# Performance work log

Hardware: AMD Instinct MI355X
Metric: run time of the kernel (lower is better)

The kernel has to match this reference:

```python
import jax, jax.numpy as jnp
import numpy as np

NUM_SAMPLES = 8192   # num_parallel_samples
HIDDEN = 512
EMB = 40             # embedding_dim(10) * freq_map['H'](4)
C_IN = 1
TIME_FEAT = 4
HIST_LEN = 336
PRED_LEN = 48
MIN_SCALE = 1e-5
SAMPLE_KEY_SEED = 42


def _gru_cell(h, x, W_ih, W_hh, b_ih, b_hh):
    # torch GRU cell: gates stacked as [r, z, n] along rows of W (each HIDDEN)
    gi = x @ W_ih.T + b_ih            # [B, 3H]
    gh = h @ W_hh.T + b_hh            # [B, 3H]
    H = h.shape[-1]
    i_r, i_z, i_n = gi[:, :H], gi[:, H:2 * H], gi[:, 2 * H:]
    h_r, h_z, h_n = gh[:, :H], gh[:, H:2 * H], gh[:, 2 * H:]
    r = jax.nn.sigmoid(i_r + h_r)
    z = jax.nn.sigmoid(i_z + h_z)
    n = jnp.tanh(i_n + r * h_n)
    return (1.0 - z) * n + z * h


def setup_inputs() -> dict:
    key = jax.random.key(0)
    ks = jax.random.split(key, 16)
    f32 = jnp.float32
    inp = {
        "x": jax.random.normal(ks[0], (1, HIST_LEN, C_IN), dtype=f32),
        "x_mark": jax.random.normal(ks[1], (1, HIST_LEN, TIME_FEAT), dtype=f32),
        "y_mark": jax.random.normal(ks[2], (1, PRED_LEN, TIME_FEAT), dtype=f32),
        "mode": 0,
        # time_feat_embedding: Linear(4 -> 40), torch layout [out, in]
        "W_emb": jax.random.normal(ks[3], (EMB, TIME_FEAT), dtype=f32) * 0.05,
        "b_emb": jnp.zeros((EMB,), dtype=f32),
        # GRU (1 layer): input size = c_in + EMB = 41
        "W_ih": jax.random.normal(ks[4], (3 * HIDDEN, C_IN + EMB), dtype=f32) * 0.05,
        "W_hh": jax.random.normal(ks[5], (3 * HIDDEN, HIDDEN), dtype=f32) * 0.05,
        "b_ih": jnp.zeros((3 * HIDDEN,), dtype=f32),
        "b_hh": jnp.zeros((3 * HIDDEN,), dtype=f32),
        # StudentT args projection: three Linear(HIDDEN -> 1)
        "W_df": jax.random.normal(ks[6], (1, HIDDEN), dtype=f32) * 0.05,
        "b_df": jnp.zeros((1,), dtype=f32),
        "W_loc": jax.random.normal(ks[7], (1, HIDDEN), dtype=f32) * 0.05,
        "b_loc": jnp.zeros((1,), dtype=f32),
        "W_sc": jax.random.normal(ks[8], (1, HIDDEN), dtype=f32) * 0.05,
        "b_sc": jnp.zeros((1,), dtype=f32),
    }
    return inp


def _deepar_sample(x, x_mark, y_mark, W_emb, b_emb, W_ih, W_hh, b_ih, b_hh,
                   W_df, b_df, W_loc, b_loc, W_sc, b_sc):
    S = NUM_SAMPLES
    # ---- encoder (unroll_encoder with y=None) ----
    scale = jnp.clip(jnp.mean(jnp.abs(x), axis=1, keepdims=True), MIN_SCALE, None)  # [1,1,1]
    seq = x / scale
    tfe = x_mark @ W_emb.T + b_emb                      # [1, T, EMB]
    enc_in = jnp.concatenate([seq, tfe], axis=-1)       # [1, T, 41]
    h0 = jnp.zeros((1, HIDDEN), dtype=x.dtype)

    def enc_step(h, xt):  # xt: [1, 41]
        h = _gru_cell(h, xt, W_ih, W_hh, b_ih, b_hh)
        return h, None

    h_T, _ = jax.lax.scan(enc_step, h0, jnp.swapaxes(enc_in, 0, 1))  # [1, H]

    # ---- sampling decoder ----
    h = jnp.broadcast_to(h_T, (S, HIDDEN))              # repeat state across samples
    # note: original feeds the UNSCALED last observation as first decoder input
    tgt0 = jnp.broadcast_to(x[0, -1, :], (S, C_IN))     # [S, 1]
    emb_y = y_mark[0] @ W_emb.T + b_emb                 # [pred_len, EMB]
    scale_s = scale[0, 0, 0]                            # scalar (batch=1, c=1)
    base_key = jax.random.key(SAMPLE_KEY_SEED)

    def dec_step(carry, xs):
        h, tgt = carry
        e_k, k = xs
        inp = jnp.concatenate([tgt, jnp.broadcast_to(e_k, (S, EMB))], axis=-1)  # [S, 41]
        h = _gru_cell(h, inp, W_ih, W_hh, b_ih, b_hh)
        # StudentTOutput domain map: df = 2 + softplus, loc raw, scale = softplus
        df = 2.0 + jax.nn.softplus(h @ W_df.T + b_df)   # [S, 1]
        loc = h @ W_loc.T + b_loc                       # [S, 1]
        sc = jax.nn.softplus(h @ W_sc.T + b_sc)         # [S, 1]
        eps = jax.random.t(jax.random.fold_in(base_key, k),
                           jax.lax.stop_gradient(df), df.shape, dtype=df.dtype)
        sample = (loc + sc * eps) * scale_s             # AffineTransformed(scale)
        return (h, sample), sample

    ks = jnp.arange(PRED_LEN)
    _, samples = jax.lax.scan(dec_step, (h, tgt0), (emb_y, ks))  # [pred_len, S, 1]
    return jnp.transpose(samples, (1, 0, 2))            # [S, pred_len, c_out]


def reference(x, x_mark, y_mark, mode, W_emb, b_emb, W_ih, W_hh, b_ih, b_hh,
              W_df, b_df, W_loc, b_loc, W_sc, b_sc):
    # mode=0 -> sampling/inference path (the kernel target)
    return _deepar_sample(x, x_mark, y_mark, W_emb, b_emb, W_ih, W_hh, b_ih, b_hh,
                          W_df, b_df, W_loc, b_loc, W_sc, b_sc)
```

## Files before the change

### kernel.cpp

```cpp
#include <hip/hip_runtime.h>
#include <cmath>


#define JAX_PARTITIONABLE 1

#define HIDDEN 512
#define EMB 40
#define HIST 336
#define PRED 48
#define S_N 8192
#define ENC_BLOCKS 48

#define HPLANE (8192 * 512)
#define WPLANE (1536 * 512)
#define INV4096 (1.0f / 4096.0f)

typedef __attribute__((ext_vector_type(8))) _Float16 half8;
typedef __attribute__((ext_vector_type(4))) float f32x4;

struct KeyPair { unsigned a, b; };

__device__ __forceinline__ unsigned rotl32_(unsigned v, unsigned s) {
  return (v << s) | (v >> (32u - s));
}

__device__ __forceinline__ KeyPair tf2x32(KeyPair k, unsigned x0, unsigned x1) {
  unsigned ks0 = k.a, ks1 = k.b, ks2 = ks0 ^ ks1 ^ 0x1BD11BDAu;
  x0 += ks0; x1 += ks1;
#define TF_R(r) { x0 += x1; x1 = rotl32_(x1, r); x1 ^= x0; }
  TF_R(13u) TF_R(15u) TF_R(26u) TF_R(6u)  x0 += ks1; x1 += ks2 + 1u;
  TF_R(17u) TF_R(29u) TF_R(16u) TF_R(24u) x0 += ks2; x1 += ks0 + 2u;
  TF_R(13u) TF_R(15u) TF_R(26u) TF_R(6u)  x0 += ks0; x1 += ks1 + 3u;
  TF_R(17u) TF_R(29u) TF_R(16u) TF_R(24u) x0 += ks1; x1 += ks2 + 4u;
  TF_R(13u) TF_R(15u) TF_R(26u) TF_R(6u)  x0 += ks2; x1 += ks0 + 5u;
#undef TF_R
  KeyPair r; r.a = x0; r.b = x1; return r;
}

__device__ __forceinline__ void split2_(KeyPair key, KeyPair& r0, KeyPair& r1) {
#if JAX_PARTITIONABLE
  r0 = tf2x32(key, 0u, 0u);
  r1 = tf2x32(key, 0u, 1u);
#else
  KeyPair p0 = tf2x32(key, 0u, 2u);
  KeyPair p1 = tf2x32(key, 1u, 3u);
  r0.a = p0.a; r0.b = p1.a;
  r1.a = p0.b; r1.b = p1.b;
#endif
}

__device__ __forceinline__ void split3_(KeyPair key, KeyPair& r0, KeyPair& r1, KeyPair& r2) {
#if JAX_PARTITIONABLE
  r0 = tf2x32(key, 0u, 0u);
  r1 = tf2x32(key, 0u, 1u);
  r2 = tf2x32(key, 0u, 2u);
#else
  KeyPair p0 = tf2x32(key, 0u, 3u);
  KeyPair p1 = tf2x32(key, 1u, 4u);
  KeyPair p2 = tf2x32(key, 2u, 5u);
  r0.a = p0.a; r0.b = p1.a;
  r1.a = p2.a; r1.b = p0.b;
  r2.a = p1.b; r2.b = p2.b;
#endif
}

__device__ __forceinline__ unsigned scalar_bits_(KeyPair key) {
#if JAX_PARTITIONABLE
  KeyPair p = tf2x32(key, 0u, 0u);
  return p.a ^ p.b;
#else
  return tf2x32(key, 0u, 0u).a;
#endif
}

__device__ __forceinline__ unsigned batch_bits_8192_(KeyPair key, int s) {
#if JAX_PARTITIONABLE
  KeyPair p = tf2x32(key, 0u, (unsigned)s);
  return p.a ^ p.b;
#else
  if (s < 4096) return tf2x32(key, (unsigned)s, (unsigned)(4096 + s)).a;
  return tf2x32(key, (unsigned)(s - 4096), (unsigned)s).b;
#endif
}

__device__ __forceinline__ KeyPair subkey_of_8192_(KeyPair key, int s) {
#if JAX_PARTITIONABLE
  return tf2x32(key, 0u, (unsigned)s);
#else
  KeyPair r;
  if (s < 4096) {
    r.a = tf2x32(key, (unsigned)(2 * s),     (unsigned)(8192 + 2 * s)).a;
    r.b = tf2x32(key, (unsigned)(2 * s + 1), (unsigned)(8192 + 2 * s + 1)).a;
  } else {
    int m = 2 * s - 8192;
    r.a = tf2x32(key, (unsigned)m,       (unsigned)(m + 8192)).b;
    r.b = tf2x32(key, (unsigned)(m + 1), (unsigned)(m + 1 + 8192)).b;
  }
  return r;
#endif
}

__device__ __forceinline__ float acc_logf_(float x) {
  return (float)log((double)x);
}
__device__ __forceinline__ float acc_expf_(float x) {
  return (float)exp((double)x);
}

__device__ __forceinline__ float bits_to_uniform01_(unsigned bits) {
  return __uint_as_float((bits >> 9) | 0x3F800000u) - 1.0f;
}

__device__ __forceinline__ float xla_log1pf_(float t) {
  #pragma clang fp contract(off)
  float small_ = (1.0f + (-0.5f) * t) * t;
  float large_ = acc_logf_(t + 1.0f);
  return (fabsf(t) < 1e-4f) ? small_ : large_;
}

__device__ float xla_erfinv_(float x) {
  #pragma clang fp contract(off)
  float w = -xla_log1pf_(-(x * x));
  float p;
  if (w < 5.0f) {
    float ww = w - 2.5f;
    p = 2.81022636e-08f;
    p = 3.43273939e-07f + p * ww;
    p = -3.5233877e-06f + p * ww;
    p = -4.39150654e-06f + p * ww;
    p = 0.00021858087f + p * ww;
    p = -0.00125372503f + p * ww;
    p = -0.00417768164f + p * ww;
    p = 0.246640727f + p * ww;
    p = 1.50140941f + p * ww;
  } else {
    float ww = sqrtf(w) - 3.0f;
    p = -0.000200214257f;
    p = 0.000100950558f + p * ww;
    p = 0.00134934322f + p * ww;
    p = -0.00367342844f + p * ww;
    p = 0.00573950773f + p * ww;
    p = -0.0076224613f + p * ww;
    p = 0.00943887047f + p * ww;
    p = 1.00167406f + p * ww;
    p = 2.83297682f + p * ww;
  }
  return p * x;
}

__device__ float bits_to_normal_(unsigned bits) {
  #pragma clang fp contract(off)
  const float lo = __uint_as_float(0xBF7FFFFFu);
  float f = bits_to_uniform01_(bits);
  float u = f * 2.0f + lo;
  u = fmaxf(lo, u);
  return __uint_as_float(0x3FB504F3u) * xla_erfinv_(u);
}

__device__ __forceinline__ float softplus_(float x) {
  #pragma clang fp contract(off)
  float amax = fmaxf(x, 0.0f);
  float e = acc_expf_(-fabsf(x));
  return amax + xla_log1pf_(e);
}

__device__ __forceinline__ float sigmoid_(float v) { return 1.0f / (1.0f + expf(-v)); }

__device__ __forceinline__ unsigned short f2h_(float f) {
  _Float16 h = (_Float16)f;
  return __builtin_bit_cast(unsigned short, h);
}
__device__ __forceinline__ float h2f_(unsigned short b) {
  return (float)__builtin_bit_cast(_Float16, b);
}

__device__ float gamma_sample_(KeyPair gkey, float alpha) {
  #pragma clang fp contract(off)
  const float third = 0.33333334f;
  float d = alpha - third;
  float c = third / sqrtf(d);
  KeyPair key, boost_sub;
  split2_(gkey, key, boost_sub);
  (void)boost_sub;
  float X = 0.0f, V = 1.0f, U = 2.0f;
  for (int guard = 0; guard < 1024; guard++) {
    float X2 = X * X;
    float sq = 1.0f - 0.0331f * (X2 * X2);
    bool cont = false;
    if (U >= sq) {
      float lhs = acc_logf_(U);
      float rhs = (X * 0.5f) + (d * ((1.0f - V) + acc_logf_(V)));
      cont = (lhs >= rhs);
    }
    if (!cont) break;
    KeyPair nkey, xkey, Ukey;
    split3_(key, nkey, xkey, Ukey);
    key = nkey;
    float x, v;
    KeyPair kk = xkey;
    do {
      KeyPair knew, sub;
      split2_(kk, knew, sub);
      kk = knew;
      x = bits_to_normal_(scalar_bits_(sub));
      v = 1.0f + x * c;
    } while (v <= 0.0f);
    X = x * x;
    V = (v * v) * v;
    U = bits_to_uniform01_(scalar_bits_(Ukey));
  }
  return d * V;
}

__device__ float sample_t_eps_(int k, int s, float df) {
  #pragma clang fp contract(off)
  KeyPair base; base.a = 0u; base.b = 42u;
  KeyPair tkey = tf2x32(base, 0u, (unsigned)k);
  KeyPair key_n, key_g;
  split2_(tkey, key_n, key_g);
  float n = bits_to_normal_(batch_bits_8192_(key_n, s));
  KeyPair gkey = subkey_of_8192_(key_g, s);
  float half_df = df * 0.5f;
  float g = gamma_sample_(gkey, half_df);
  return n * sqrtf(half_df / g);
}


__global__ __launch_bounds__(256) void prep_kernel(
    const float* __restrict__ x, const float* __restrict__ x_mark,
    const float* __restrict__ y_mark, const float* __restrict__ W_emb,
    const float* __restrict__ b_emb, float* __restrict__ scale_p,
    float* __restrict__ tfe, float* __restrict__ emb_y,
    unsigned long long* __restrict__ gh2) {
  __shared__ float xs[HIST];
  int tid = threadIdx.x;
  for (int i = tid; i < HIST; i += 256) xs[i] = fabsf(x[i]);
  __syncthreads();
  if (tid == 0) {
    float s = 0.0f;
    for (int t = 0; t < HIST; t++) s += xs[t];
    float m = s / 336.0f;
    scale_p[0] = fmaxf(m, 1e-5f);
  }
  for (int i = tid; i < 2 * 1536; i += 256) gh2[i] = 0ull;
  for (int idx = tid; idx < HIST * EMB; idx += 256) {
    int t = idx / EMB, e = idx % EMB;
    float a = b_emb[e];
    for (int f = 0; f < 4; f++) a += x_mark[t * 4 + f] * W_emb[e * 4 + f];
    tfe[idx] = a;
  }
  for (int idx = tid; idx < PRED * EMB; idx += 256) {
    int kk = idx / EMB, e = idx % EMB;
    float a = b_emb[e];
    for (int f = 0; f < 4; f++) a += y_mark[kk * 4 + f] * W_emb[e * 4 + f];
    emb_y[idx] = a;
  }
}

__global__ __launch_bounds__(256) void enc_gi_kernel(
    const float* __restrict__ x, const float* __restrict__ tfe,
    const float* __restrict__ W_ih, const float* __restrict__ b_ih,
    const float* __restrict__ scale_p, float* __restrict__ enc_gi) {
  __shared__ float fe[EMB];
  __shared__ float xs_s;
  int t = blockIdx.x;
  int tid = threadIdx.x;
  if (tid < EMB) fe[tid] = tfe[t * EMB + tid];
  if (tid == 0) xs_s = x[t] / scale_p[0];
  __syncthreads();
  float xs = xs_s;
  for (int r = tid; r < 3 * HIDDEN; r += 256) {
    const float* wr = W_ih + (size_t)r * 41;
    float a = b_ih[r] + wr[0] * xs;
    #pragma unroll
    for (int e = 0; e < EMB; e++) a += wr[1 + e] * fe[e];
    enc_gi[(size_t)t * 1536 + r] = a;
  }
}

__global__ __launch_bounds__(256) void giy_kernel(
    const float* __restrict__ emb_y, const float* __restrict__ W_ih,
    const float* __restrict__ b_ih, float* __restrict__ giy) {
  __shared__ float fe[EMB];
  int k = blockIdx.x;
  int tid = threadIdx.x;
  if (tid < EMB) fe[tid] = emb_y[k * EMB + tid];
  __syncthreads();
  for (int r = tid; r < 3 * HIDDEN; r += 256) {
    const float* wr = W_ih + (size_t)r * 41;
    float a = b_ih[r];
    #pragma unroll
    for (int e = 0; e < EMB; e++) a += wr[1 + e] * fe[e];
    giy[(size_t)k * 1536 + r] = a;
  }
}

__global__ __launch_bounds__(256) void wsplit_kernel(
    const float* __restrict__ W_hh, unsigned short* __restrict__ Wr) {
  int row = blockIdx.x;
  int g = row >> 9;
  int jg = row & 511;
  int jb = jg >> 5, jl = jg & 31;
  size_t dst = ((size_t)jb * 96 + g * 32 + jl) * 512;
  for (int k = threadIdx.x; k < 512; k += 256) {
    float w = W_hh[(size_t)row * 512 + k];
    unsigned short g0 = f2h_(w);
    float r1 = (w - h2f_(g0)) * 4096.0f;
    unsigned short g1 = f2h_(r1);
    Wr[dst + k] = g0;
    Wr[WPLANE + dst + k] = g1;
  }
}

__global__ __launch_bounds__(256) void hsplit_kernel(
    const float* __restrict__ h_T, unsigned short* __restrict__ sT) {
  int i = threadIdx.x;
  for (int j = i; j < 512; j += 256) {
    float v = h_T[j];
    unsigned short f0 = f2h_(v);
    float r1 = (v - h2f_(f0)) * 4096.0f;
    sT[j] = f0;
    sT[512 + j] = f2h_(r1);
  }
}

__global__ __launch_bounds__(128) void h2bcast_kernel(
    const unsigned short* __restrict__ sT, unsigned short* __restrict__ h2) {
  int row = blockIdx.x;
  int tid = threadIdx.x;
  int sp = tid >> 6, c = tid & 63;
  ((uint4*)(h2 + (size_t)sp * HPLANE + (size_t)row * 512))[c] =
      ((const uint4*)(sT + sp * 512))[c];
}

__device__ __forceinline__ int hpad_(int j) { return (j >> 6) * 68 + (j & 63); }

__global__ __launch_bounds__(256) void enc_gru_kernel(
    const float* __restrict__ enc_gi, const float* __restrict__ W_hh,
    const float* __restrict__ b_hh, unsigned long long* __restrict__ gh2,
    float* __restrict__ h_T) {
  __shared__ __align__(16) float hsb[2][544];
  int tid = threadIdx.x;
  int gtid = blockIdx.x * 256 + tid;
  int row = gtid >> 3;
  int sub = gtid & 7;

  float w[64];
  const float* wp = W_hh + (size_t)row * HIDDEN + sub * 64;
  #pragma unroll
  for (int i = 0; i < 16; i++) {
    float4 v = *(const float4*)(wp + 4 * i);
    w[4 * i + 0] = v.x; w[4 * i + 1] = v.y; w[4 * i + 2] = v.z; w[4 * i + 3] = v.w;
  }
  for (int i = tid; i < 544; i += 256) hsb[0][i] = 0.f;
  float bhr0 = b_hh[tid],       bhz0 = b_hh[512 + tid],  bhn0 = b_hh[1024 + tid];
  float bhr1 = b_hh[256 + tid], bhz1 = b_hh[768 + tid],  bhn1 = b_hh[1280 + tid];
  __syncthreads();

  for (int t = 0; t < HIST; t++) {
    int par = t & 1;
    unsigned tag = (unsigned)(t + 1);
    const float* hc = hsb[par];
    float* hw = hsb[par ^ 1];

    const float* gi = enc_gi + (size_t)t * 1536;
    float gir0 = gi[tid],        giz0 = gi[512 + tid],  gin0 = gi[1024 + tid];
    float gir1 = gi[256 + tid],  giz1 = gi[768 + tid],  gin1 = gi[1280 + tid];

    float p = 0.0f;
    const float4* hv = (const float4*)(hc + sub * 68);
    #pragma unroll
    for (int i = 0; i < 16; i++) {
      float4 v = hv[i];
      p += w[4 * i + 0] * v.x + w[4 * i + 1] * v.y +
           w[4 * i + 2] * v.z + w[4 * i + 3] * v.w;
    }
    p += __shfl_xor(p, 1, 64);
    p += __shfl_xor(p, 2, 64);
    p += __shfl_xor(p, 4, 64);
    if (sub == 0) {
      unsigned long long pk =
          ((unsigned long long)tag << 32) | (unsigned long long)__float_as_uint(p);
      __hip_atomic_store(&gh2[par * 1536 + row], pk, __ATOMIC_RELAXED,
                         __HIP_MEMORY_SCOPE_AGENT);
    }

    const unsigned long long* g = gh2 + par * 1536;
    unsigned long long v0, v1, v2, v3, v4, v5;
    for (;;) {
      v0 = __hip_atomic_load(&g[tid],         __ATOMIC_RELAXED, __HIP_MEMORY_SCOPE_AGENT);
      v1 = __hip_atomic_load(&g[512 + tid],   __ATOMIC_RELAXED, __HIP_MEMORY_SCOPE_AGENT);
      v2 = __hip_atomic_load(&g[1024 + tid],  __ATOMIC_RELAXED, __HIP_MEMORY_SCOPE_AGENT);
      v3 = __hip_atomic_load(&g[256 + tid],   __ATOMIC_RELAXED, __HIP_MEMORY_SCOPE_AGENT);
      v4 = __hip_atomic_load(&g[768 + tid],   __ATOMIC_RELAXED, __HIP_MEMORY_SCOPE_AGENT);
      v5 = __hip_atomic_load(&g[1280 + tid],  __ATOMIC_RELAXED, __HIP_MEMORY_SCOPE_AGENT);
      if ((unsigned)(v0 >> 32) == tag && (unsigned)(v1 >> 32) == tag &&
          (unsigned)(v2 >> 32) == tag && (unsigned)(v3 >> 32) == tag &&
          (unsigned)(v4 >> 32) == tag && (unsigned)(v5 >> 32) == tag)
        break;
      __builtin_amdgcn_s_sleep(1);
    }

    {
      float ghr = __uint_as_float((unsigned)v0);
      float ghz = __uint_as_float((unsigned)v1);
      float ghn = __uint_as_float((unsigned)v2);
      float r = sigmoid_(gir0 + (ghr + bhr0));
      float z = sigmoid_(giz0 + (ghz + bhz0));
      float n = tanhf(gin0 + r * (ghn + bhn0));
      hw[hpad_(tid)] = (1.0f - z) * n + z * hc[hpad_(tid)];
    }
    {
      float ghr = __uint_as_float((unsigned)v3);
      float ghz = __uint_as_float((unsigned)v4);
      float ghn = __uint_as_float((unsigned)v5);
      float r = sigmoid_(gir1 + (ghr + bhr1));
      float z = sigmoid_(giz1 + (ghz + bhz1));
      float n = tanhf(gin1 + r * (ghn + bhn1));
      hw[hpad_(tid + 256)] = (1.0f - z) * n + z * hc[hpad_(tid + 256)];
    }
    __syncthreads();
  }
  if (blockIdx.x == 0) {
    h_T[tid] = hsb[0][hpad_(tid)];
    h_T[tid + 256] = hsb[0][hpad_(tid + 256)];
  }
}

__global__ __launch_bounds__(256, 2) void dec_gru_mfma(
    const unsigned short* __restrict__ h2_in,
    const unsigned short* __restrict__ Wr,
    const float* __restrict__ giy_k, const float* __restrict__ b_hh,
    const float* __restrict__ W_ih, const float* __restrict__ tgt,
    int tgt_is_x, unsigned short* __restrict__ h2_out,
    const float* __restrict__ W_df, const float* __restrict__ W_loc,
    const float* __restrict__ W_sc, float* __restrict__ partials) {
  __shared__ unsigned short As[2][2][128][32];
  int b_ = blockIdx.x;
  int xcd = b_ & 7, slot = b_ >> 3;
  int mb = xcd * 8 + (slot & 7);
  int jb = slot >> 3;
  int tid = threadIdx.x;
  int lane = tid & 63;
  int wave = tid >> 6;
  int wm = wave >> 1, wn = wave & 1;
  int s0 = mb * 128;
  int q = lane >> 4, c = lane & 15;

  f32x4 accm[4][3], accc[4][3];
  #pragma unroll
  for (int i = 0; i < 4; i++)
    #pragma unroll
    for (int g = 0; g < 3; g++) {
      accm[i][g] = (f32x4){0.f, 0.f, 0.f, 0.f};
      accc[i][g] = (f32x4){0.f, 0.f, 0.f, 0.f};
    }

  float hold[4][4];
  #pragma unroll
  for (int i = 0; i < 4; i++)
    #pragma unroll
    for (int r = 0; r < 4; r++) hold[i][r] = 0.f;

  int asp[4], arow[4], acol[4];
  #pragma unroll
  for (int r = 0; r < 4; r++) {
    int a = r * 256 + tid;
    asp[r] = a >> 9;
    int rem = a & 511;
    arow[r] = rem >> 2;
    acol[r] = rem & 3;
  }

  const unsigned short* Bbase =
      Wr + ((size_t)jb * 96 + wn * 16 + c) * 512 + q * 8;

  #pragma unroll
  for (int r = 0; r < 4; r++) {
    uint4 v = *(const uint4*)(h2_in + (size_t)asp[r] * HPLANE +
                              (size_t)(s0 + arow[r]) * 512 + acol[r] * 8);
    *(uint4*)&As[0][asp[r]][arow[r]][(acol[r] ^ (arow[r] & 3)) * 8] = v;
  }
  half8 Bcur[3][2];
  #pragma unroll
  for (int g = 0; g < 3; g++) {
    Bcur[g][0] = *(const half8*)(Bbase + (size_t)g * 32 * 512);
    Bcur[g][1] = *(const half8*)(Bbase + WPLANE + (size_t)g * 32 * 512);
  }
  __syncthreads();

  int cur = 0;
  for (int kbi = 0; kbi < 16; kbi++) {
    int kb = kbi * 32;
    uint4 Areg[4];
    half8 Bn[3][2];
    if (kbi < 15) {
      #pragma unroll
      for (int r = 0; r < 4; r++)
        Areg[r] = *(const uint4*)(h2_in + (size_t)asp[r] * HPLANE +
                                  (size_t)(s0 + arow[r]) * 512 + kb + 32 +
                                  acol[r] * 8);
      #pragma unroll
      for (int g = 0; g < 3; g++) {
        Bn[g][0] = *(const half8*)(Bbase + (size_t)g * 32 * 512 + kb + 32);
        Bn[g][1] = *(const half8*)(Bbase + WPLANE + (size_t)g * 32 * 512 + kb + 32);
      }
    }
    if (kbi == jb) {
      int cc = wn * 16 + c;
      #pragma unroll
      for (int i = 0; i < 4; i++)
        #pragma unroll
        for (int reg = 0; reg < 4; reg++) {
          int m = wm * 64 + i * 16 + q * 4 + reg;
          int idx = (((cc >> 3) ^ (m & 3)) << 3) + (cc & 7);
          hold[i][reg] = h2f_(As[cur][0][m][idx]) +
                         h2f_(As[cur][1][m][idx]) * INV4096;
        }
    }
    #pragma unroll
    for (int i = 0; i < 4; i++) {
      int m = wm * 64 + i * 16 + c;
      half8 a0 = *(const half8*)&As[cur][0][m][(q ^ (c & 3)) * 8];
      half8 a1 = *(const half8*)&As[cur][1][m][(q ^ (c & 3)) * 8];
      #pragma unroll
      for (int g = 0; g < 3; g++) {
        accm[i][g] = __builtin_amdgcn_mfma_f32_16x16x32_f16(a0, Bcur[g][0], accm[i][g], 0, 0, 0);
        accc[i][g] = __builtin_amdgcn_mfma_f32_16x16x32_f16(a0, Bcur[g][1], accc[i][g], 0, 0, 0);
        accc[i][g] = __builtin_amdgcn_mfma_f32_16x16x32_f16(a1, Bcur[g][0], accc[i][g], 0, 0, 0);
      }
    }
    if (kbi < 15) {
      #pragma unroll
      for (int r = 0; r < 4; r++)
        *(uint4*)&As[cur ^ 1][asp[r]][arow[r]][(acol[r] ^ (arow[r] & 3)) * 8] =
            Areg[r];
      #pragma unroll
      for (int g = 0; g < 3; g++) {
        Bcur[g][0] = Bn[g][0];
        Bcur[g][1] = Bn[g][1];
      }
    }
    __syncthreads();
    cur ^= 1;
  }

  float* pb = (float*)&As[0][0][0][0];
  {
    int j = jb * 32 + wn * 16 + c;
    float gyr = giy_k[j], gyz = giy_k[512 + j], gyn = giy_k[1024 + j];
    float w0r = W_ih[(size_t)j * 41];
    float w0z = W_ih[(size_t)(512 + j) * 41];
    float w0n = W_ih[(size_t)(1024 + j) * 41];
    float bhr = b_hh[j], bhz = b_hh[512 + j], bhn = b_hh[1024 + j];
    float wdj = W_df[j], wlj = W_loc[j], wsj = W_sc[j];
    #pragma unroll
    for (int i = 0; i < 4; i++) {
      #pragma unroll
      for (int reg = 0; reg < 4; reg++) {
        int s = s0 + wm * 64 + i * 16 + q * 4 + reg;
        float tg = tgt_is_x ? tgt[HIST - 1] : tgt[s];
        size_t off = (size_t)s * 512 + j;
        float h_old = hold[i][reg];
        float ghr = accm[i][0][reg] + accc[i][0][reg] * INV4096;
        float ghz = accm[i][1][reg] + accc[i][1][reg] * INV4096;
        float ghn = accm[i][2][reg] + accc[i][2][reg] * INV4096;
        float gr = (gyr + w0r * tg) + (ghr + bhr);
        float gz = (gyz + w0z * tg) + (ghz + bhz);
        float gn_i = gyn + w0n * tg;
        float gn_h = ghn + bhn;
        float r_ = sigmoid_(gr);
        float z_ = sigmoid_(gz);
        float n_ = tanhf(gn_i + r_ * gn_h);
        float hn = (1.0f - z_) * n_ + z_ * h_old;
        unsigned short f0 = f2h_(hn);
        float r1 = (hn - h2f_(f0)) * 4096.0f;
        __builtin_nontemporal_store(f0, &h2_out[off]);
        __builtin_nontemporal_store(f2h_(r1), &h2_out[HPLANE + off]);
        float vd = hn * wdj, vl = hn * wlj, vs = hn * wsj;
        #pragma unroll
        for (int o = 1; o < 16; o <<= 1) {
          vd += __shfl_xor(vd, o, 64);
          vl += __shfl_xor(vl, o, 64);
          vs += __shfl_xor(vs, o, 64);
        }
        if (c == 0) {
          int sl = i * 16 + q * 4 + reg;
          int bix = ((wm * 2 + wn) * 64 + sl) * 3;
          pb[bix + 0] = vd; pb[bix + 1] = vl; pb[bix + 2] = vs;
        }
      }
    }
  }
  __syncthreads();
  if (tid < 128) {
    int wmh = tid >> 6, sl = tid & 63;
    int ia = (wmh * 2 + 0) * 192 + sl * 3;
    int ib = ia + 192;
    int s = s0 + wmh * 64 + sl;
    size_t pofs = (size_t)s * 48 + jb * 3;
    partials[pofs + 0] = pb[ia + 0] + pb[ib + 0];
    partials[pofs + 1] = pb[ia + 1] + pb[ib + 1];
    partials[pofs + 2] = pb[ia + 2] + pb[ib + 2];
  }
}

__global__ __launch_bounds__(64) void dec_head_kernel(
    const float* __restrict__ partials, const float* __restrict__ b_df,
    const float* __restrict__ b_loc, const float* __restrict__ b_sc,
    const float* __restrict__ scale_p, float* __restrict__ tgt,
    float* __restrict__ out, int k) {
  #pragma clang fp contract(off)
  int s = blockIdx.x * 64 + threadIdx.x;
  const float* p = partials + (size_t)s * 48;
  float adf = 0.f, alo = 0.f, asc = 0.f;
  #pragma unroll
  for (int jb = 0; jb < 16; jb++) {
    adf += p[jb * 3 + 0];
    alo += p[jb * 3 + 1];
    asc += p[jb * 3 + 2];
  }
  float df = 2.0f + softplus_(adf + b_df[0]);
  float loc = alo + b_loc[0];
  float sc = softplus_(asc + b_sc[0]);
  float eps = sample_t_eps_(k, s, df);
  float smp = (loc + sc * eps) * scale_p[0];
  out[(size_t)s * PRED + k] = smp;
  tgt[s] = smp;
}

extern "C" void kernel_launch(void* const* d_in, const int* in_sizes, int n_in,
                              void* d_out, int out_size, void* d_ws, size_t ws_size,
                              hipStream_t stream) {
  const float* x      = (const float*)d_in[0];
  const float* x_mark = (const float*)d_in[1];
  const float* y_mark = (const float*)d_in[2];
  const float* W_emb  = (const float*)d_in[4];
  const float* b_emb  = (const float*)d_in[5];
  const float* W_ih   = (const float*)d_in[6];
  const float* W_hh   = (const float*)d_in[7];
  const float* b_ih   = (const float*)d_in[8];
  const float* b_hh   = (const float*)d_in[9];
  const float* W_df   = (const float*)d_in[10];
  const float* b_df   = (const float*)d_in[11];
  const float* W_loc  = (const float*)d_in[12];
  const float* b_loc  = (const float*)d_in[13];
  const float* W_sc   = (const float*)d_in[14];
  const float* b_sc   = (const float*)d_in[15];
  float* out = (float*)d_out;

  float* w = (float*)d_ws;
  unsigned short* h2_a = (unsigned short*)(w);
  unsigned short* h2_b = (unsigned short*)(w + 4194304);
  unsigned short* Wr   = (unsigned short*)(w + 8388608);
  float* enc_gi = w + 9175040;
  float* giy    = w + 9691136;
  float* tfe    = w + 9764864;
  float* emb_y  = w + 9778304;
  unsigned long long* gh2 = (unsigned long long*)(w + 9780224);
  float* h_T    = w + 9786368;
  unsigned short* sT = (unsigned short*)(w + 9786880);
  float* tgt    = w + 9787392;
  float* scale_p = w + 9795584;
  float* partials = w + 9795588;

  prep_kernel<<<1, 256, 0, stream>>>(x, x_mark, y_mark, W_emb, b_emb,
                                     scale_p, tfe, emb_y, gh2);
  enc_gi_kernel<<<HIST, 256, 0, stream>>>(x, tfe, W_ih, b_ih, scale_p, enc_gi);
  giy_kernel<<<PRED, 256, 0, stream>>>(emb_y, W_ih, b_ih, giy);
  wsplit_kernel<<<1536, 256, 0, stream>>>(W_hh, Wr);
  enc_gru_kernel<<<ENC_BLOCKS, 256, 0, stream>>>(enc_gi, W_hh, b_hh, gh2, h_T);
  hsplit_kernel<<<1, 256, 0, stream>>>(h_T, sT);
  h2bcast_kernel<<<S_N, 128, 0, stream>>>(sT, h2_a);

  for (int k = 0; k < PRED; k++) {
    const unsigned short* h_in = (k % 2 == 0) ? h2_a : h2_b;
    unsigned short* h_o = (k % 2 == 0) ? h2_b : h2_a;
    dec_gru_mfma<<<1024, 256, 0, stream>>>(
        h_in, Wr, giy + (size_t)k * 1536, b_hh, W_ih,
        (k == 0) ? x : tgt, (k == 0) ? 1 : 0, h_o,
        W_df, W_loc, W_sc, partials);
    dec_head_kernel<<<S_N / 64, 64, 0, stream>>>(
        partials, b_df, b_loc, b_sc, scale_p, tgt, out, k);
  }
}
```

Before: 5.034 ms.

## Fuse decoder steps into one persistent kernel with grid barrier and tagged targets

Replaces the 96 per-step launches (GRU MFMA step plus head kernel) with a single persistent kernel of 512 blocks. Each block handles two tiles per step and meets the others at a software grid barrier built from arrive flags and a go flag. The head/sampling phase for step k-1 runs on 32 blocks at the start of step k and publishes targets tagged with the step index. GRU blocks spin on those tags only after their matmul, which overlaps the head with the recurrent GEMM. This removes launch overhead and inter-kernel gaps, but it relies on all 512 blocks being co-resident (2 per CU) and adds spin-wait traffic.

Result: slower. 6.960 ms (+38.3%).

```diff
diff --git a/kernel.cpp b/kernel.cpp
--- a/kernel.cpp
+++ b/kernel.cpp
@@ -10,6 +10,7 @@
 #define PRED 48
 #define S_N 8192
 #define ENC_BLOCKS 48
+#define DEC_BLOCKS 512
 
 #define HPLANE (8192 * 512)
 #define WPLANE (1536 * 512)
@@ -231,7 +232,10 @@
     const float* __restrict__ y_mark, const float* __restrict__ W_emb,
     const float* __restrict__ b_emb, float* __restrict__ scale_p,
     float* __restrict__ tfe, float* __restrict__ emb_y,
-    unsigned long long* __restrict__ gh2) {
+    unsigned long long* __restrict__ gh2,
+    unsigned long long* __restrict__ tgt2,
+    unsigned long long* __restrict__ arrive,
+    unsigned long long* __restrict__ goflag) {
   __shared__ float xs[HIST];
   int tid = threadIdx.x;
   for (int i = tid; i < HIST; i += 256) xs[i] = fabsf(x[i]);
@@ -243,6 +247,9 @@
     scale_p[0] = fmaxf(m, 1e-5f);
   }
   for (int i = tid; i < 2 * 1536; i += 256) gh2[i] = 0ull;
+  for (int i = tid; i < S_N; i += 256) tgt2[i] = 0ull;
+  for (int i = tid; i < DEC_BLOCKS; i += 256) arrive[i] = 0ull;
+  if (tid == 0) goflag[0] = 0ull;
   for (int idx = tid; idx < HIST * EMB; idx += 256) {
     int t = idx / EMB, e = idx % EMB;
     float a = b_emb[e];
@@ -427,16 +434,14 @@
   }
 }
 
-__global__ __launch_bounds__(256, 2) void dec_gru_mfma(
-    const unsigned short* __restrict__ h2_in,
-    const unsigned short* __restrict__ Wr,
-    const float* __restrict__ giy_k, const float* __restrict__ b_hh,
-    const float* __restrict__ W_ih, const float* __restrict__ tgt,
-    int tgt_is_x, unsigned short* __restrict__ h2_out,
-    const float* __restrict__ W_df, const float* __restrict__ W_loc,
-    const float* __restrict__ W_sc, float* __restrict__ partials) {
-  __shared__ unsigned short As[2][2][128][32];
-  int b_ = blockIdx.x;
+__device__ void dec_slot_(
+    int b_, int k, const unsigned short* __restrict__ h2_in,
+    const unsigned short* __restrict__ Wr, const float* __restrict__ giy_k,
+    const float* __restrict__ b_hh, const float* __restrict__ W_ih,
+    float xlast, const unsigned long long* __restrict__ tgt2,
+    unsigned short* __restrict__ h2_out, const float* __restrict__ W_df,
+    const float* __restrict__ W_loc, const float* __restrict__ W_sc,
+    float* __restrict__ partials, unsigned short (*As)[2][128][32]) {
   int xcd = b_ & 7, slot = b_ >> 3;
   int mb = xcd * 8 + (slot & 7);
   int jb = slot >> 3;
@@ -543,6 +548,31 @@
     }
     __syncthreads();
     cur ^= 1;
+  }
+
+  float tgv[4][4];
+  if (k == 0) {
+    #pragma unroll
+    for (int i = 0; i < 4; i++)
+      #pragma unroll
+      for (int reg = 0; reg < 4; reg++) tgv[i][reg] = xlast;
+  } else {
+    unsigned tagk = (unsigned)k;
+    for (;;) {
+      bool ok = true;
+      #pragma unroll
+      for (int i = 0; i < 4; i++)
+        #pragma unroll
+        for (int reg = 0; reg < 4; reg++) {
+          int s = s0 + wm * 64 + i * 16 + q * 4 + reg;
+          unsigned long long v = __hip_atomic_load(&tgt2[s], __ATOMIC_RELAXED,
+                                                   __HIP_MEMORY_SCOPE_AGENT);
+          ok &= ((unsigned)(v >> 32) == tagk);
+          tgv[i][reg] = __uint_as_float((unsigned)v);
+        }
+      if (ok) break;
+      __builtin_amdgcn_s_sleep(1);
+    }
   }
 
   float* pb = (float*)&As[0][0][0][0];
@@ -559,7 +589,7 @@
       #pragma unroll
       for (int reg = 0; reg < 4; reg++) {
         int s = s0 + wm * 64 + i * 16 + q * 4 + reg;
-        float tg = tgt_is_x ? tgt[HIST - 1] : tgt[s];
+        float tg = tgv[i][reg];
         size_t off = (size_t)s * 512 + j;
         float h_old = hold[i][reg];
         float ghr = accm[i][0][reg] + accc[i][0][reg] * INV4096;
@@ -605,20 +635,20 @@
   }
 }
 
-__global__ __launch_bounds__(64) void dec_head_kernel(
-    const float* __restrict__ partials, const float* __restrict__ b_df,
-    const float* __restrict__ b_loc, const float* __restrict__ b_sc,
-    const float* __restrict__ scale_p, float* __restrict__ tgt,
-    float* __restrict__ out, int k) {
+__device__ void head_phase_(
+    int p, int tid, int k, const float* __restrict__ partials,
+    const float* __restrict__ b_df, const float* __restrict__ b_loc,
+    const float* __restrict__ b_sc, const float* __restrict__ scale_p,
+    unsigned long long* __restrict__ tgt2, float* __restrict__ out) {
   #pragma clang fp contract(off)
-  int s = blockIdx.x * 64 + threadIdx.x;
-  const float* p = partials + (size_t)s * 48;
+  int s = p * 256 + tid;
+  const float* pp = partials + (size_t)s * 48;
   float adf = 0.f, alo = 0.f, asc = 0.f;
   #pragma unroll
   for (int jb = 0; jb < 16; jb++) {
-    adf += p[jb * 3 + 0];
-    alo += p[jb * 3 + 1];
-    asc += p[jb * 3 + 2];
+    adf += pp[jb * 3 + 0];
+    alo += pp[jb * 3 + 1];
+    asc += pp[jb * 3 + 2];
   }
   float df = 2.0f + softplus_(adf + b_df[0]);
   float loc = alo + b_loc[0];
@@ -626,7 +656,73 @@
   float eps = sample_t_eps_(k, s, df);
   float smp = (loc + sc * eps) * scale_p[0];
   out[(size_t)s * PRED + k] = smp;
-  tgt[s] = smp;
+  unsigned long long pk = ((unsigned long long)(unsigned)(k + 1) << 32) |
+                          (unsigned long long)__float_as_uint(smp);
+  __hip_atomic_store(&tgt2[s], pk, __ATOMIC_RELAXED, __HIP_MEMORY_SCOPE_AGENT);
+}
+
+__global__ __launch_bounds__(256, 2) void dec_persist_kernel(
+    unsigned short* __restrict__ h2_a, unsigned short* __restrict__ h2_b,
+    const unsigned short* __restrict__ Wr, const float* __restrict__ giy,
+    const float* __restrict__ b_hh, const float* __restrict__ W_ih,
+    const float* __restrict__ x, const float* __restrict__ W_df,
+    const float* __restrict__ W_loc, const float* __restrict__ W_sc,
+    float* __restrict__ partials, const float* __restrict__ b_df,
+    const float* __restrict__ b_loc, const float* __restrict__ b_sc,
+    const float* __restrict__ scale_p, float* __restrict__ out,
+    unsigned long long* __restrict__ tgt2,
+    unsigned long long* __restrict__ arrive,
+    unsigned long long* __restrict__ goflag) {
+  __shared__ unsigned short As[2][2][128][32];
+  int p = blockIdx.x;
+  int tid = threadIdx.x;
+  float xlast = x[HIST - 1];
+
+  for (int k = 0; k < PRED; k++) {
+    if (p < 32 && k > 0)
+      head_phase_(p, tid, k - 1, partials, b_df, b_loc, b_sc, scale_p, tgt2, out);
+
+    const unsigned short* h_in = (k & 1) ? h2_b : h2_a;
+    unsigned short* h_o = (k & 1) ? h2_a : h2_b;
+    const float* giy_k = giy + (size_t)k * 1536;
+
+    dec_slot_(p, k, h_in, Wr, giy_k, b_hh, W_ih, xlast, tgt2, h_o,
+              W_df, W_loc, W_sc, partials, As);
+    __syncthreads();
+    dec_slot_(p + 512, k, h_in, Wr, giy_k, b_hh, W_ih, xlast, tgt2, h_o,
+              W_df, W_loc, W_sc, partials, As);
+    __syncthreads();
+
+    unsigned long long gen = (unsigned long long)(k + 1);
+    if (tid == 0)
+      __hip_atomic_store(&arrive[p], gen, __ATOMIC_RELEASE,
+                         __HIP_MEMORY_SCOPE_AGENT);
+    if (p == 0) {
+      for (;;) {
+        unsigned long long a0 = __hip_atomic_load(&arrive[tid], __ATOMIC_RELAXED,
+                                                  __HIP_MEMORY_SCOPE_AGENT);
+        unsigned long long a1 = __hip_atomic_load(&arrive[tid + 256],
+                                                  __ATOMIC_RELAXED,
+                                                  __HIP_MEMORY_SCOPE_AGENT);
+        if (a0 >= gen && a1 >= gen) break;
+        __builtin_amdgcn_s_sleep(1);
+      }
+      __syncthreads();
+      if (tid == 0)
+        __hip_atomic_store(goflag, gen, __ATOMIC_RELEASE,
+                           __HIP_MEMORY_SCOPE_AGENT);
+    }
+    for (;;) {
+      unsigned long long g = __hip_atomic_load(goflag, __ATOMIC_RELAXED,
+                                               __HIP_MEMORY_SCOPE_AGENT);
+      if (g >= gen) break;
+      __builtin_amdgcn_s_sleep(1);
+    }
+    (void)__hip_atomic_load(goflag, __ATOMIC_ACQUIRE, __HIP_MEMORY_SCOPE_AGENT);
+    __syncthreads();
+  }
+  if (p < 32)
+    head_phase_(p, tid, PRED - 1, partials, b_df, b_loc, b_sc, scale_p, tgt2, out);
 }
 
 extern "C" void kernel_launch(void* const* d_in, const int* in_sizes, int n_in,
@@ -660,12 +756,15 @@
   unsigned long long* gh2 = (unsigned long long*)(w + 9780224);
   float* h_T    = w + 9786368;
   unsigned short* sT = (unsigned short*)(w + 9786880);
-  float* tgt    = w + 9787392;
-  float* scale_p = w + 9795584;
-  float* partials = w + 9795588;
+  float* scale_p = w + 9787392;
+  float* partials = w + 9787396;
+  unsigned long long* tgt2 = (unsigned long long*)(w + 10180612);
+  unsigned long long* arrive = (unsigned long long*)(w + 10196996);
+  unsigned long long* goflag = (unsigned long long*)(w + 10198020);
 
   prep_kernel<<<1, 256, 0, stream>>>(x, x_mark, y_mark, W_emb, b_emb,
-                                     scale_p, tfe, emb_y, gh2);
+                                     scale_p, tfe, emb_y, gh2, tgt2, arrive,
+                                     goflag);
   enc_gi_kernel<<<HIST, 256, 0, stream>>>(x, tfe, W_ih, b_ih, scale_p, enc_gi);
   giy_kernel<<<PRED, 256, 0, stream>>>(emb_y, W_ih, b_ih, giy);
   wsplit_kernel<<<1536, 256, 0, stream>>>(W_hh, Wr);
@@ -673,14 +772,7 @@
   hsplit_kernel<<<1, 256, 0, stream>>>(h_T, sT);
   h2bcast_kernel<<<S_N, 128, 0, stream>>>(sT, h2_a);
 
-  for (int k = 0; k < PRED; k++) {
-    const unsigned short* h_in = (k % 2 == 0) ? h2_a : h2_b;
-    unsigned short* h_o = (k % 2 == 0) ? h2_b : h2_a;
-    dec_gru_mfma<<<1024, 256, 0, stream>>>(
-        h_in, Wr, giy + (size_t)k * 1536, b_hh, W_ih,
-        (k == 0) ? x : tgt, (k == 0) ? 1 : 0, h_o,
-        W_df, W_loc, W_sc, partials);
-    dec_head_kernel<<<S_N / 64, 64, 0, stream>>>(
-        partials, b_df, b_loc, b_sc, scale_p, tgt, out, k);
-  }
-}
+  dec_persist_kernel<<<DEC_BLOCKS, 256, 0, stream>>>(
+      h2_a, h2_b, Wr, giy, b_hh, W_ih, x, W_df, W_loc, W_sc,
+      partials, b_df, b_loc, b_sc, scale_p, out, tgt2, arrive, goflag);
+}
```

## Fuse decoder head into next-step GRU kernel and improve LDS swizzle

Applied to the files above, without the earlier changes.

Folds the per-step StudentT head (reducing partials, sampling eps, writing output) into the prologue of the next step's GRU MFMA kernel. Each of the 16 column blocks recomputes the samples for its 128 rows and keeps them in shared memory. This removes 48 small head launches and the tgt round-trip through global memory, at the cost of 16x redundant head work and a second ping-pong partials buffer that reuses the enc_gi region. It also adds an extra XOR term to the LDS swizzle to cut bank conflicts and raises launch_bounds occupancy to 4 blocks per CU.

After: 12.57 ms. 150% more time.

```diff
diff --git a/kernel.cpp b/kernel.cpp
--- a/kernel.cpp
+++ b/kernel.cpp
@@ -427,15 +427,46 @@
   }
 }
 
-__global__ __launch_bounds__(256, 2) void dec_gru_mfma(
+__device__ void head_prologue_(
+    int mb, int jb, int tid, int kk, const float* __restrict__ partials_prev,
+    const float* __restrict__ b_df, const float* __restrict__ b_loc,
+    const float* __restrict__ b_sc, const float* __restrict__ scale_p,
+    float* __restrict__ out, float* __restrict__ tgLds) {
+  #pragma clang fp contract(off)
+  if (tid < 128) {
+    int s = mb * 128 + tid;
+    const float* pp = partials_prev + (size_t)s * 48;
+    float adf = 0.f, alo = 0.f, asc = 0.f;
+    #pragma unroll
+    for (int jbx = 0; jbx < 16; jbx++) {
+      adf += pp[jbx * 3 + 0];
+      alo += pp[jbx * 3 + 1];
+      asc += pp[jbx * 3 + 2];
+    }
+    float df = 2.0f + softplus_(adf + b_df[0]);
+    float loc = alo + b_loc[0];
+    float sc = softplus_(asc + b_sc[0]);
+    float eps = sample_t_eps_(kk, s, df);
+    float smp = (loc + sc * eps) * scale_p[0];
+    tgLds[tid] = smp;
+    if (jb == 0) out[(size_t)s * PRED + kk] = smp;
+  }
+}
+
+__global__ __launch_bounds__(256, 4) void dec_fused_kernel(
     const unsigned short* __restrict__ h2_in,
     const unsigned short* __restrict__ Wr,
     const float* __restrict__ giy_k, const float* __restrict__ b_hh,
-    const float* __restrict__ W_ih, const float* __restrict__ tgt,
-    int tgt_is_x, unsigned short* __restrict__ h2_out,
+    const float* __restrict__ W_ih, const float* __restrict__ x, int k,
+    unsigned short* __restrict__ h2_out,
     const float* __restrict__ W_df, const float* __restrict__ W_loc,
-    const float* __restrict__ W_sc, float* __restrict__ partials) {
+    const float* __restrict__ W_sc,
+    const float* __restrict__ partials_prev, float* __restrict__ partials_out,
+    const float* __restrict__ b_df, const float* __restrict__ b_loc,
+    const float* __restrict__ b_sc, const float* __restrict__ scale_p,
+    float* __restrict__ out) {
   __shared__ unsigned short As[2][2][128][32];
+  __shared__ float tgLds[128];
   int b_ = blockIdx.x;
   int xcd = b_ & 7, slot = b_ >> 3;
   int mb = xcd * 8 + (slot & 7);
@@ -447,6 +478,11 @@
   int s0 = mb * 128;
   int q = lane >> 4, c = lane & 15;
 
+  if (k > 0)
+    head_prologue_(mb, jb, tid, k - 1, partials_prev, b_df, b_loc, b_sc,
+                   scale_p, out, tgLds);
+  float xlast = x[HIST - 1];
+
   f32x4 accm[4][3], accc[4][3];
   #pragma unroll
   for (int i = 0; i < 4; i++)
@@ -475,11 +511,14 @@
   const unsigned short* Bbase =
       Wr + ((size_t)jb * 96 + wn * 16 + c) * 512 + q * 8;
 
+  int rdsw = (q ^ (c & 3) ^ (c >> 2)) * 8;
+
   #pragma unroll
   for (int r = 0; r < 4; r++) {
     uint4 v = *(const uint4*)(h2_in + (size_t)asp[r] * HPLANE +
                               (size_t)(s0 + arow[r]) * 512 + acol[r] * 8);
-    *(uint4*)&As[0][asp[r]][arow[r]][(acol[r] ^ (arow[r] & 3)) * 8] = v;
+    *(uint4*)&As[0][asp[r]][arow[r]]
+        [(acol[r] ^ (arow[r] & 3) ^ ((arow[r] >> 2) & 3)) * 8] = v;
   }
   half8 Bcur[3][2];
   #pragma unroll
@@ -513,7 +552,7 @@
         #pragma unroll
         for (int reg = 0; reg < 4; reg++) {
           int m = wm * 64 + i * 16 + q * 4 + reg;
-          int idx = (((cc >> 3) ^ (m & 3)) << 3) + (cc & 7);
+          int idx = (((cc >> 3) ^ reg ^ q) << 3) + (cc & 7);
           hold[i][reg] = h2f_(As[cur][0][m][idx]) +
                          h2f_(As[cur][1][m][idx]) * INV4096;
         }
@@ -521,8 +560,8 @@
     #pragma unroll
     for (int i = 0; i < 4; i++) {
       int m = wm * 64 + i * 16 + c;
-      half8 a0 = *(const half8*)&As[cur][0][m][(q ^ (c & 3)) * 8];
-      half8 a1 = *(const half8*)&As[cur][1][m][(q ^ (c & 3)) * 8];
+      half8 a0 = *(const half8*)&As[cur][0][m][rdsw];
+      half8 a1 = *(const half8*)&As[cur][1][m][rdsw];
       #pragma unroll
       for (int g = 0; g < 3; g++) {
         accm[i][g] = __builtin_amdgcn_mfma_f32_16x16x32_f16(a0, Bcur[g][0], accm[i][g], 0, 0, 0);
@@ -533,8 +572,8 @@
     if (kbi < 15) {
       #pragma unroll
       for (int r = 0; r < 4; r++)
-        *(uint4*)&As[cur ^ 1][asp[r]][arow[r]][(acol[r] ^ (arow[r] & 3)) * 8] =
-            Areg[r];
+        *(uint4*)&As[cur ^ 1][asp[r]][arow[r]]
+            [(acol[r] ^ (arow[r] & 3) ^ ((arow[r] >> 2) & 3)) * 8] = Areg[r];
       #pragma unroll
       for (int g = 0; g < 3; g++) {
         Bcur[g][0] = Bn[g][0];
@@ -559,7 +598,7 @@
       #pragma unroll
       for (int reg = 0; reg < 4; reg++) {
         int s = s0 + wm * 64 + i * 16 + q * 4 + reg;
-        float tg = tgt_is_x ? tgt[HIST - 1] : tgt[s];
+        float tg = (k == 0) ? xlast : tgLds[wm * 64 + i * 16 + q * 4 + reg];
         size_t off = (size_t)s * 512 + j;
         float h_old = hold[i][reg];
         float ghr = accm[i][0][reg] + accc[i][0][reg] * INV4096;
@@ -599,17 +638,16 @@
     int ib = ia + 192;
     int s = s0 + wmh * 64 + sl;
     size_t pofs = (size_t)s * 48 + jb * 3;
-    partials[pofs + 0] = pb[ia + 0] + pb[ib + 0];
-    partials[pofs + 1] = pb[ia + 1] + pb[ib + 1];
-    partials[pofs + 2] = pb[ia + 2] + pb[ib + 2];
-  }
-}
-
-__global__ __launch_bounds__(64) void dec_head_kernel(
+    partials_out[pofs + 0] = pb[ia + 0] + pb[ib + 0];
+    partials_out[pofs + 1] = pb[ia + 1] + pb[ib + 1];
+    partials_out[pofs + 2] = pb[ia + 2] + pb[ib + 2];
+  }
+}
+
+__global__ __launch_bounds__(64) void dec_head_final(
     const float* __restrict__ partials, const float* __restrict__ b_df,
     const float* __restrict__ b_loc, const float* __restrict__ b_sc,
-    const float* __restrict__ scale_p, float* __restrict__ tgt,
-    float* __restrict__ out, int k) {
+    const float* __restrict__ scale_p, float* __restrict__ out) {
   #pragma clang fp contract(off)
   int s = blockIdx.x * 64 + threadIdx.x;
   const float* p = partials + (size_t)s * 48;
@@ -623,10 +661,9 @@
   float df = 2.0f + softplus_(adf + b_df[0]);
   float loc = alo + b_loc[0];
   float sc = softplus_(asc + b_sc[0]);
-  float eps = sample_t_eps_(k, s, df);
+  float eps = sample_t_eps_(PRED - 1, s, df);
   float smp = (loc + sc * eps) * scale_p[0];
-  out[(size_t)s * PRED + k] = smp;
-  tgt[s] = smp;
+  out[(size_t)s * PRED + (PRED - 1)] = smp;
 }
 
 extern "C" void kernel_launch(void* const* d_in, const int* in_sizes, int n_in,
@@ -660,9 +697,9 @@
   unsigned long long* gh2 = (unsigned long long*)(w + 9780224);
   float* h_T    = w + 9786368;
   unsigned short* sT = (unsigned short*)(w + 9786880);
-  float* tgt    = w + 9787392;
   float* scale_p = w + 9795584;
-  float* partials = w + 9795588;
+  float* partials0 = w + 9795588;
+  float* partials1 = enc_gi;
 
   prep_kernel<<<1, 256, 0, stream>>>(x, x_mark, y_mark, W_emb, b_emb,
                                      scale_p, tfe, emb_y, gh2);
@@ -674,13 +711,14 @@
   h2bcast_kernel<<<S_N, 128, 0, stream>>>(sT, h2_a);
 
   for (int k = 0; k < PRED; k++) {
-    const unsigned short* h_in = (k % 2 == 0) ? h2_a : h2_b;
-    unsigned short* h_o = (k % 2 == 0) ? h2_b : h2_a;
-    dec_gru_mfma<<<1024, 256, 0, stream>>>(
-        h_in, Wr, giy + (size_t)k * 1536, b_hh, W_ih,
-        (k == 0) ? x : tgt, (k == 0) ? 1 : 0, h_o,
-        W_df, W_loc, W_sc, partials);
-    dec_head_kernel<<<S_N / 64, 64, 0, stream>>>(
-        partials, b_df, b_loc, b_sc, scale_p, tgt, out, k);
-  }
-}
+    const unsigned short* h_in = (k & 1) ? h2_b : h2_a;
+    unsigned short* h_o = (k & 1) ? h2_a : h2_b;
+    const float* pprev = (k & 1) ? partials0 : partials1;
+    float* pcur = (k & 1) ? partials1 : partials0;
+    dec_fused_kernel<<<1024, 256, 0, stream>>>(
+        h_in, Wr, giy + (size_t)k * 1536, b_hh, W_ih, x, k, h_o,
+        W_df, W_loc, W_sc, pprev, pcur, b_df, b_loc, b_sc, scale_p, out);
+  }
+  dec_head_final<<<S_N / 64, 64, 0, stream>>>(partials1, b_df, b_loc, b_sc,
+                                              scale_p, out);
+}
```
